# Kernel optimization log

Hardware: AMD Instinct MI355X
Metric: run time of the kernel (lower is better)

Reference implementation:

```python
import jax, jax.numpy as jnp
import numpy as np

BITS = 4
N_PACK = 8  # 32-bit container / 4-bit values
GROUPSIZE = 128
MASK = (1 << BITS) - 1


def _unpack(packed, n_valid):
    # packed: [R, ceil(n_valid/N_PACK)] int32 -> [R, n_valid] int32 nibbles
    shifts = (jnp.arange(N_PACK, dtype=jnp.int32) * BITS)
    vals = (packed[:, :, None] >> shifts) & MASK  # [R, C, N_PACK]
    return vals.reshape(packed.shape[0], -1)[:, :n_valid]


def setup_inputs() -> dict:
    key = jax.random.key(0)
    k0, k1, k2, k3, k4 = jax.random.split(key, 5)
    O, I = 4096, 4096
    ng = I // GROUPSIZE  # 32
    x = jax.random.normal(k0, (2, 2048, I), dtype=jnp.float32)
    packed_weight = jax.random.randint(k1, (O, I // N_PACK), 0, 2147483647, dtype=jnp.int32)
    scale = jax.random.uniform(k2, (O, ng), dtype=jnp.float32)
    packed_zp = jax.random.randint(k3, (O, (ng + N_PACK - 1) // N_PACK), 0, 2147483647, dtype=jnp.int32)
    bias = jax.random.normal(k4, (O,), dtype=jnp.float32)
    return {"x": x, "packed_weight": packed_weight, "scale": scale,
            "packed_zp": packed_zp, "bias": bias}


def reference(x, packed_weight, scale, packed_zp, bias):
    O, ng = scale.shape
    I = packed_weight.shape[1] * N_PACK
    # unpack uint4 weights and zero-points (matches torch recover(): shift+mask)
    w_int = _unpack(packed_weight, I)          # [O, I] values in [0, 15]
    zp_int = _unpack(packed_zp, ng)            # [O, ng]
    # per-group dequant: (w - zp) * scale
    w = w_int.reshape(O, ng, GROUPSIZE).astype(scale.dtype)
    fp_weight = ((w - zp_int[:, :, None].astype(scale.dtype)) * scale[:, :, None]).reshape(O, I)
    # F.linear: x @ W^T + b
    return jnp.einsum('bsi,oi->bso', x, fp_weight) + bias
```

## Files before the change

### kernel.cpp

```cpp
#include <hip/hip_runtime.h>
#include <stdint.h>

typedef __attribute__((ext_vector_type(4))) float  floatx4;
typedef __attribute__((ext_vector_type(8))) short  shortx8;
typedef __attribute__((ext_vector_type(4))) unsigned short ushortx4;

typedef unsigned int   u32;
typedef unsigned short u16;

#define TILE    128
#define BK      64
#define THREADS 256
#define CHUNK   (TILE * BK)

__device__ __forceinline__ u32 pack2bf(float f0, float f1) {
    u32 u0 = __builtin_bit_cast(u32, f0) + 0x8000u;
    u32 u1 = __builtin_bit_cast(u32, f1) + 0x8000u;
    return __builtin_amdgcn_perm(u1, u0, 0x07060302u);
}

__device__ __forceinline__ unsigned short f2bf(float f) {
    u32 u = __builtin_bit_cast(u32, f);
    u += 0x7FFFu + ((u >> 16) & 1u);
    return (unsigned short)(u >> 16);
}

__global__ __launch_bounds__(THREADS)
void prep_kernel(const float* __restrict__ x, const int* __restrict__ pw,
                 const float* __restrict__ scale, const int* __restrict__ pzp,
                 u16* __restrict__ At, u16* __restrict__ Bt,
                 int M, int O, int I, int ng, int KT) {
    const int bid = blockIdx.x;
    const int t   = threadIdx.x;
    if (bid < M * 2) {
        const int row  = bid >> 1;
        const int cseg = (bid & 1) * THREADS + t;
        const int kt = cseg >> 3, cp = cseg & 7;
        const int r = row & (TILE - 1), mt = row >> 7;
        const int c = cp ^ (r & 7);
        const float4 v0 = *(const float4*)(x + (size_t)row * I + kt * BK + c * 8);
        const float4 v1 = *(const float4*)(x + (size_t)row * I + kt * BK + c * 8 + 4);
        u32 p[4];
        p[0] = pack2bf(v0.x, v0.y);
        p[1] = pack2bf(v0.z, v0.w);
        p[2] = pack2bf(v1.x, v1.y);
        p[3] = pack2bf(v1.z, v1.w);
        *(uint4*)(At + (size_t)(mt * KT + kt) * CHUNK + r * BK + cp * 8) = *(uint4*)p;
    } else {
        const int bid2 = bid - M * 2;
        const int o    = bid2 >> 1;
        const int wpos = (bid2 & 1) * THREADS + t;
        const int kt = wpos >> 3, cp = wpos & 7;
        const int r = o & (TILE - 1), nt = o >> 7;
        const int c = cp ^ (r & 7);
        const u32 wq = (u32)pw[(size_t)o * (I >> 3) + kt * 8 + c];
        const int g  = (kt * BK) / (I / ng);
        const float s = scale[o * ng + g];
        const int zpw = pzp[o * ((ng + 7) >> 3) + (g >> 3)];
        const int zp  = (zpw >> ((g & 7) * 4)) & 15;
        const float nzc = -s * (float)(zp + 128);
        float v[8];
        #pragma unroll
        for (int j = 0; j < 8; j++) {
            u32 tt;
            if (j < 4)       tt = (wq << (16 - 4 * j)) & 0x000F0000u;
            else if (j == 4) tt = wq & 0x000F0000u;
            else             tt = (wq >> (4 * j - 16)) & 0x000F0000u;
            float f = __builtin_bit_cast(float, tt | 0x43000000u);
            v[j] = __builtin_fmaf(f, s, nzc);
        }
        u32 p[4];
        p[0] = pack2bf(v[0], v[1]);
        p[1] = pack2bf(v[2], v[3]);
        p[2] = pack2bf(v[4], v[5]);
        p[3] = pack2bf(v[6], v[7]);
        *(uint4*)(Bt + (size_t)(nt * KT + kt) * CHUNK + r * BK + cp * 8) = *(uint4*)p;
    }
}

__global__ __launch_bounds__(THREADS, 2)
void gemm_bf16(const u16* __restrict__ At, const u16* __restrict__ Bt,
               const float* __restrict__ bias, float* __restrict__ out,
               int O, int KT) {
    __shared__ u16 As[CHUNK];
    __shared__ u16 Bs[CHUNK];

    const int tid = threadIdx.x;
    const int nblk_n = O / TILE;
    const int mt = blockIdx.x / nblk_n;
    const int nt = blockIdx.x % nblk_n;
    const int w = tid >> 6, lane = tid & 63;
    const int wm = w >> 1, wn = w & 1;
    const int l15 = lane & 15, l4 = lane >> 4;
    const int sw  = l15 & 7;

    floatx4 acc[4][4];
    #pragma unroll
    for (int i = 0; i < 4; i++)
        #pragma unroll
        for (int j = 0; j < 4; j++)
            acc[i][j] = (floatx4){0.f, 0.f, 0.f, 0.f};

    for (int kt = 0; kt < KT; kt++) {
        const u16* ga = At + (size_t)(mt * KT + kt) * CHUNK;
        const u16* gb = Bt + (size_t)(nt * KT + kt) * CHUNK;
        __syncthreads();
        #pragma unroll
        for (int it = 0; it < 4; it++) {
            const int off = (it * THREADS + tid) * 8;
            __builtin_amdgcn_global_load_lds((const __attribute__((address_space(1))) u32*)(ga + off),
                                             (__attribute__((address_space(3))) u32*)(As + off),
                                             16, 0, 0);
            __builtin_amdgcn_global_load_lds((const __attribute__((address_space(1))) u32*)(gb + off),
                                             (__attribute__((address_space(3))) u32*)(Bs + off),
                                             16, 0, 0);
        }
        __syncthreads();

        #pragma unroll
        for (int ks = 0; ks < 2; ks++) {
            shortx8 af[4], bf[4];
            #pragma unroll
            for (int i = 0; i < 4; i++)
                af[i] = *(const shortx8*)(&As[(wm * 64 + i * 16 + l15) * BK + ((ks * 4 + l4) ^ sw) * 8]);
            #pragma unroll
            for (int j = 0; j < 4; j++)
                bf[j] = *(const shortx8*)(&Bs[(wn * 64 + j * 16 + l15) * BK + ((ks * 4 + l4) ^ sw) * 8]);
            #pragma unroll
            for (int i = 0; i < 4; i++)
                #pragma unroll
                for (int j = 0; j < 4; j++)
                    acc[i][j] = __builtin_amdgcn_mfma_f32_16x16x32_bf16(af[i], bf[j], acc[i][j], 0, 0, 0);
        }
    }

    #pragma unroll
    for (int j = 0; j < 4; j++) {
        int col  = nt * TILE + wn * 64 + j * 16 + l15;
        float bv = bias[col];
        #pragma unroll
        for (int i = 0; i < 4; i++) {
            int rowb = mt * TILE + wm * 64 + i * 16 + l4 * 4;
            #pragma unroll
            for (int r = 0; r < 4; r++)
                out[(size_t)(rowb + r) * O + col] = acc[i][j][r] + bv;
        }
    }
}

#define LDA 72
__global__ __launch_bounds__(THREADS, 2)
void wql_fused(const float* __restrict__ x, const int* __restrict__ pw,
               const float* __restrict__ scale, const int* __restrict__ pzp,
               const float* __restrict__ bias, float* __restrict__ out,
               int M, int O, int I, int ng)
{
    __shared__ unsigned short As[TILE * LDA];
    __shared__ unsigned short Bs[TILE * LDA];
    const int tid = threadIdx.x;
    const int nblk_n = O / TILE;
    const int mt = blockIdx.x / nblk_n, nt = blockIdx.x % nblk_n;
    const int w = tid >> 6, lane = tid & 63;
    const int wm = w >> 1, wn = w & 1;
    const int l15 = lane & 15, l4 = lane >> 4;
    const int pw_rowlen = I / 8, zp_rowlen = (ng + 7) / 8, GS = I / ng;

    floatx4 acc[4][4];
    #pragma unroll
    for (int i = 0; i < 4; i++)
        #pragma unroll
        for (int j = 0; j < 4; j++) acc[i][j] = (floatx4){0.f, 0.f, 0.f, 0.f};

    const int nk = I / BK;
    for (int kt = 0; kt < nk; kt++) {
        __syncthreads();
        #pragma unroll
        for (int it = 0; it < 8; it++) {
            int f = tid + it * THREADS;
            int row = f >> 4, seg = f & 15;
            const float4 v = *(const float4*)(x + (size_t)(mt * TILE + row) * I + kt * BK + seg * 4);
            ushortx4 b;
            b.x = f2bf(v.x); b.y = f2bf(v.y); b.z = f2bf(v.z); b.w = f2bf(v.w);
            *(ushortx4*)(&As[row * LDA + seg * 4]) = b;
        }
        const int g = (kt * BK) / GS;
        #pragma unroll
        for (int it = 0; it < 4; it++) {
            int e = tid + it * THREADS;
            int row = e >> 3, c = e & 7;
            int o = nt * TILE + row;
            int wq = pw[(size_t)o * pw_rowlen + kt * (BK / 8) + c];
            float s = scale[o * ng + g];
            int zpw = pzp[o * zp_rowlen + (g >> 3)];
            int zp = (zpw >> ((g & 7) * 4)) & 15;
            shortx8 b;
            #pragma unroll
            for (int j = 0; j < 8; j++) {
                int nib = (wq >> (4 * j)) & 15;
                b[j] = (short)f2bf((float)(nib - zp) * s);
            }
            *(shortx8*)(&Bs[row * LDA + c * 8]) = b;
        }
        __syncthreads();
        #pragma unroll
        for (int ks = 0; ks < 2; ks++) {
            shortx8 af[4], bf[4];
            #pragma unroll
            for (int i = 0; i < 4; i++)
                af[i] = *(const shortx8*)(&As[(wm * 64 + i * 16 + l15) * LDA + ks * 32 + l4 * 8]);
            #pragma unroll
            for (int j = 0; j < 4; j++)
                bf[j] = *(const shortx8*)(&Bs[(wn * 64 + j * 16 + l15) * LDA + ks * 32 + l4 * 8]);
            #pragma unroll
            for (int i = 0; i < 4; i++)
                #pragma unroll
                for (int j = 0; j < 4; j++)
                    acc[i][j] = __builtin_amdgcn_mfma_f32_16x16x32_bf16(af[i], bf[j], acc[i][j], 0, 0, 0);
        }
    }
    #pragma unroll
    for (int j = 0; j < 4; j++) {
        int col = nt * TILE + wn * 64 + j * 16 + l15;
        float bv = bias[col];
        #pragma unroll
        for (int i = 0; i < 4; i++) {
            int rowb = mt * TILE + wm * 64 + i * 16 + l4 * 4;
            #pragma unroll
            for (int r = 0; r < 4; r++)
                out[(size_t)(rowb + r) * O + col] = acc[i][j][r] + bv;
        }
    }
}

extern "C" void kernel_launch(void* const* d_in, const int* in_sizes, int n_in,
                              void* d_out, int out_size, void* d_ws, size_t ws_size,
                              hipStream_t stream) {
    const float* x     = (const float*)d_in[0];
    const int*   pw    = (const int*)d_in[1];
    const float* scale = (const float*)d_in[2];
    const int*   pzp   = (const int*)d_in[3];
    const float* bias  = (const float*)d_in[4];
    float*       out   = (float*)d_out;

    const int O  = in_sizes[4];
    const int ng = in_sizes[2] / O;
    const int I  = (in_sizes[1] / O) * 8;
    const int M  = in_sizes[0] / I;
    const int KT = I / BK;

    const size_t need = ((size_t)M * I + (size_t)O * I) * sizeof(u16);
    if (ws_size >= need) {
        u16* At = (u16*)d_ws;
        u16* Bt = At + (size_t)M * I;
        prep_kernel<<<dim3(M * 2 + O * 2), THREADS, 0, stream>>>(x, pw, scale, pzp, At, Bt, M, O, I, ng, KT);
        gemm_bf16<<<dim3((M / TILE) * (O / TILE)), THREADS, 0, stream>>>(At, Bt, bias, out, O, KT);
    } else {
        wql_fused<<<dim3((M / TILE) * (O / TILE)), THREADS, 0, stream>>>(x, pw, scale, pzp, bias, out, M, O, I, ng);
    }
}
```

Measured before the change: 257.6 us.

## Double-buffer GEMM LDS loads and use grid-stride prep kernel

Result: slower. 270.3 us (+4.9%).

```diff
diff --git a/kernel.cpp b/kernel.cpp
--- a/kernel.cpp
+++ b/kernel.cpp
@@ -29,36 +29,40 @@
 void prep_kernel(const float* __restrict__ x, const int* __restrict__ pw,
                  const float* __restrict__ scale, const int* __restrict__ pzp,
                  u16* __restrict__ At, u16* __restrict__ Bt,
-                 int M, int O, int I, int ng, int KT) {
-    const int bid = blockIdx.x;
-    const int t   = threadIdx.x;
-    if (bid < M * 2) {
-        const int row  = bid >> 1;
-        const int cseg = (bid & 1) * THREADS + t;
+                 int M, int O, int I, int ng, int KT, int lsSeg) {
+    const int NT = gridDim.x * THREADS;
+    const int t0 = blockIdx.x * THREADS + threadIdx.x;
+    const int segsPerRow = I >> 3;
+
+    const int Sx = M * segsPerRow;
+    for (int s = t0; s < Sx; s += NT) {
+        const int row = s >> lsSeg;
+        const int cseg = s & (segsPerRow - 1);
         const int kt = cseg >> 3, cp = cseg & 7;
         const int r = row & (TILE - 1), mt = row >> 7;
         const int c = cp ^ (r & 7);
         const float4 v0 = *(const float4*)(x + (size_t)row * I + kt * BK + c * 8);
         const float4 v1 = *(const float4*)(x + (size_t)row * I + kt * BK + c * 8 + 4);
         u32 p[4];
-        p[0] = pack2bf(v0.x, v0.y);
-        p[1] = pack2bf(v0.z, v0.w);
-        p[2] = pack2bf(v1.x, v1.y);
-        p[3] = pack2bf(v1.z, v1.w);
+        p[0] = pack2bf(v0.x, v0.y); p[1] = pack2bf(v0.z, v0.w);
+        p[2] = pack2bf(v1.x, v1.y); p[3] = pack2bf(v1.z, v1.w);
         *(uint4*)(At + (size_t)(mt * KT + kt) * CHUNK + r * BK + cp * 8) = *(uint4*)p;
-    } else {
-        const int bid2 = bid - M * 2;
-        const int o    = bid2 >> 1;
-        const int wpos = (bid2 & 1) * THREADS + t;
+    }
+
+    const int GS = I / ng;
+    const int Sw = O * segsPerRow;
+    for (int s = t0; s < Sw; s += NT) {
+        const int o = s >> lsSeg;
+        const int wpos = s & (segsPerRow - 1);
         const int kt = wpos >> 3, cp = wpos & 7;
         const int r = o & (TILE - 1), nt = o >> 7;
         const int c = cp ^ (r & 7);
-        const u32 wq = (u32)pw[(size_t)o * (I >> 3) + kt * 8 + c];
-        const int g  = (kt * BK) / (I / ng);
-        const float s = scale[o * ng + g];
+        const u32 wq = (u32)pw[(size_t)o * segsPerRow + kt * 8 + c];
+        const int g = (kt * BK) / GS;
+        const float sc = scale[o * ng + g];
         const int zpw = pzp[o * ((ng + 7) >> 3) + (g >> 3)];
-        const int zp  = (zpw >> ((g & 7) * 4)) & 15;
-        const float nzc = -s * (float)(zp + 128);
+        const int zp = (zpw >> ((g & 7) * 4)) & 15;
+        const float nzc = -sc * (float)(zp + 128);
         float v[8];
         #pragma unroll
         for (int j = 0; j < 8; j++) {
@@ -66,14 +70,11 @@
             if (j < 4)       tt = (wq << (16 - 4 * j)) & 0x000F0000u;
             else if (j == 4) tt = wq & 0x000F0000u;
             else             tt = (wq >> (4 * j - 16)) & 0x000F0000u;
-            float f = __builtin_bit_cast(float, tt | 0x43000000u);
-            v[j] = __builtin_fmaf(f, s, nzc);
+            v[j] = __builtin_fmaf(__builtin_bit_cast(float, tt | 0x43000000u), sc, nzc);
         }
         u32 p[4];
-        p[0] = pack2bf(v[0], v[1]);
-        p[1] = pack2bf(v[2], v[3]);
-        p[2] = pack2bf(v[4], v[5]);
-        p[3] = pack2bf(v[6], v[7]);
+        p[0] = pack2bf(v[0], v[1]); p[1] = pack2bf(v[2], v[3]);
+        p[2] = pack2bf(v[4], v[5]); p[3] = pack2bf(v[6], v[7]);
         *(uint4*)(Bt + (size_t)(nt * KT + kt) * CHUNK + r * BK + cp * 8) = *(uint4*)p;
     }
 }
@@ -82,8 +83,10 @@
 void gemm_bf16(const u16* __restrict__ At, const u16* __restrict__ Bt,
                const float* __restrict__ bias, float* __restrict__ out,
                int O, int KT) {
-    __shared__ u16 As[CHUNK];
-    __shared__ u16 Bs[CHUNK];
+    __shared__ u16 As0[CHUNK];
+    __shared__ u16 Bs0[CHUNK];
+    __shared__ u16 As1[CHUNK];
+    __shared__ u16 Bs1[CHUNK];
 
     const int tid = threadIdx.x;
     const int nblk_n = O / TILE;
@@ -101,38 +104,60 @@
         for (int j = 0; j < 4; j++)
             acc[i][j] = (floatx4){0.f, 0.f, 0.f, 0.f};
 
-    for (int kt = 0; kt < KT; kt++) {
-        const u16* ga = At + (size_t)(mt * KT + kt) * CHUNK;
-        const u16* gb = Bt + (size_t)(nt * KT + kt) * CHUNK;
-        __syncthreads();
-        #pragma unroll
-        for (int it = 0; it < 4; it++) {
-            const int off = (it * THREADS + tid) * 8;
-            __builtin_amdgcn_global_load_lds((const __attribute__((address_space(1))) u32*)(ga + off),
-                                             (__attribute__((address_space(3))) u32*)(As + off),
-                                             16, 0, 0);
-            __builtin_amdgcn_global_load_lds((const __attribute__((address_space(1))) u32*)(gb + off),
-                                             (__attribute__((address_space(3))) u32*)(Bs + off),
-                                             16, 0, 0);
-        }
-        __syncthreads();
-
-        #pragma unroll
-        for (int ks = 0; ks < 2; ks++) {
-            shortx8 af[4], bf[4];
-            #pragma unroll
-            for (int i = 0; i < 4; i++)
-                af[i] = *(const shortx8*)(&As[(wm * 64 + i * 16 + l15) * BK + ((ks * 4 + l4) ^ sw) * 8]);
-            #pragma unroll
-            for (int j = 0; j < 4; j++)
-                bf[j] = *(const shortx8*)(&Bs[(wn * 64 + j * 16 + l15) * BK + ((ks * 4 + l4) ^ sw) * 8]);
-            #pragma unroll
-            for (int i = 0; i < 4; i++)
-                #pragma unroll
-                for (int j = 0; j < 4; j++)
-                    acc[i][j] = __builtin_amdgcn_mfma_f32_16x16x32_bf16(af[i], bf[j], acc[i][j], 0, 0, 0);
-        }
-    }
+#define ISSUE(KTI, AS_, BS_) do {                                                              \
+    const u16* ga_ = At + (size_t)(mt * KT + (KTI)) * CHUNK;                                   \
+    const u16* gb_ = Bt + (size_t)(nt * KT + (KTI)) * CHUNK;                                   \
+    _Pragma("unroll")                                                                          \
+    for (int it_ = 0; it_ < 4; it_++) {                                                        \
+        const int off_ = (it_ * THREADS + tid) * 8;                                            \
+        __builtin_amdgcn_global_load_lds((const __attribute__((address_space(1))) u32*)(ga_ + off_), \
+                                         (__attribute__((address_space(3))) u32*)(AS_ + off_), 16, 0, 0); \
+        __builtin_amdgcn_global_load_lds((const __attribute__((address_space(1))) u32*)(gb_ + off_), \
+                                         (__attribute__((address_space(3))) u32*)(BS_ + off_), 16, 0, 0); \
+    }                                                                                          \
+} while (0)
+
+#define COMPUTE(AS_, BS_) do {                                                                 \
+    _Pragma("unroll")                                                                          \
+    for (int ks_ = 0; ks_ < 2; ks_++) {                                                        \
+        shortx8 af_[4], bf_[4];                                                                \
+        _Pragma("unroll")                                                                      \
+        for (int i_ = 0; i_ < 4; i_++)                                                         \
+            af_[i_] = *(const shortx8*)(&AS_[(wm * 64 + i_ * 16 + l15) * BK + ((ks_ * 4 + l4) ^ sw) * 8]); \
+        _Pragma("unroll")                                                                      \
+        for (int j_ = 0; j_ < 4; j_++)                                                         \
+            bf_[j_] = *(const shortx8*)(&BS_[(wn * 64 + j_ * 16 + l15) * BK + ((ks_ * 4 + l4) ^ sw) * 8]); \
+        _Pragma("unroll")                                                                      \
+        for (int i_ = 0; i_ < 4; i_++)                                                         \
+            _Pragma("unroll")                                                                  \
+            for (int j_ = 0; j_ < 4; j_++)                                                     \
+                acc[i_][j_] = __builtin_amdgcn_mfma_f32_16x16x32_bf16(af_[i_], bf_[j_], acc[i_][j_], 0, 0, 0); \
+    }                                                                                          \
+} while (0)
+
+#define WAITBAR8() __asm__ volatile("s_waitcnt vmcnt(8)\n\ts_barrier" ::: "memory")
+#define WAITBAR0() __asm__ volatile("s_waitcnt vmcnt(0)\n\ts_barrier" ::: "memory")
+#define ENDBAR()   __asm__ volatile("s_waitcnt lgkmcnt(0)\n\ts_barrier" ::: "memory")
+
+    ISSUE(0, As0, Bs0);
+    for (int kt = 0; kt < KT; kt += 2) {
+        if (kt + 1 < KT) { ISSUE(kt + 1, As1, Bs1); WAITBAR8(); }
+        else             { WAITBAR0(); }
+        COMPUTE(As0, Bs0);
+        ENDBAR();
+        if (kt + 1 < KT) {
+            if (kt + 2 < KT) { ISSUE(kt + 2, As0, Bs0); WAITBAR8(); }
+            else             { WAITBAR0(); }
+            COMPUTE(As1, Bs1);
+            ENDBAR();
+        }
+    }
+
+#undef ISSUE
+#undef COMPUTE
+#undef WAITBAR8
+#undef WAITBAR0
+#undef ENDBAR
 
     #pragma unroll
     for (int j = 0; j < 4; j++) {
@@ -247,12 +272,13 @@
     const int I  = (in_sizes[1] / O) * 8;
     const int M  = in_sizes[0] / I;
     const int KT = I / BK;
+    int lsSeg = 0; { int v = I >> 3; while ((1 << lsSeg) < v) lsSeg++; }
 
     const size_t need = ((size_t)M * I + (size_t)O * I) * sizeof(u16);
     if (ws_size >= need) {
         u16* At = (u16*)d_ws;
         u16* Bt = At + (size_t)M * I;
-        prep_kernel<<<dim3(M * 2 + O * 2), THREADS, 0, stream>>>(x, pw, scale, pzp, At, Bt, M, O, I, ng, KT);
+        prep_kernel<<<dim3(2048), THREADS, 0, stream>>>(x, pw, scale, pzp, At, Bt, M, O, I, ng, KT, lsSeg);
         gemm_bf16<<<dim3((M / TILE) * (O / TILE)), THREADS, 0, stream>>>(At, Bt, bias, out, O, KT);
     } else {
         wql_fused<<<dim3((M / TILE) * (O / TILE)), THREADS, 0, stream>>>(x, pw, scale, pzp, bias, out, M, O, I, ng);
```

## Store prepped operands row-major and apply swizzle during GEMM tile loads

Applied to the files above, without the earlier changes.

Result: no change. 257.2 us (-0.1%).

```diff
diff --git a/kernel.cpp b/kernel.cpp
--- a/kernel.cpp
+++ b/kernel.cpp
@@ -29,36 +29,31 @@
 void prep_kernel(const float* __restrict__ x, const int* __restrict__ pw,
                  const float* __restrict__ scale, const int* __restrict__ pzp,
                  u16* __restrict__ At, u16* __restrict__ Bt,
-                 int M, int O, int I, int ng, int KT) {
-    const int bid = blockIdx.x;
-    const int t   = threadIdx.x;
-    if (bid < M * 2) {
-        const int row  = bid >> 1;
-        const int cseg = (bid & 1) * THREADS + t;
-        const int kt = cseg >> 3, cp = cseg & 7;
-        const int r = row & (TILE - 1), mt = row >> 7;
-        const int c = cp ^ (r & 7);
-        const float4 v0 = *(const float4*)(x + (size_t)row * I + kt * BK + c * 8);
-        const float4 v1 = *(const float4*)(x + (size_t)row * I + kt * BK + c * 8 + 4);
+                 int M, int O, int I, int ng, int lsSeg, int lsG) {
+    const int NT = gridDim.x * THREADS;
+    const int t0 = blockIdx.x * THREADS + threadIdx.x;
+    const int segsPerRow = I >> 3;
+
+    const int Sx = (M * I) >> 3;
+    for (int s = t0; s < Sx; s += NT) {
+        const float4 v0 = ((const float4*)x)[(size_t)s * 2];
+        const float4 v1 = ((const float4*)x)[(size_t)s * 2 + 1];
         u32 p[4];
-        p[0] = pack2bf(v0.x, v0.y);
-        p[1] = pack2bf(v0.z, v0.w);
-        p[2] = pack2bf(v1.x, v1.y);
-        p[3] = pack2bf(v1.z, v1.w);
-        *(uint4*)(At + (size_t)(mt * KT + kt) * CHUNK + r * BK + cp * 8) = *(uint4*)p;
-    } else {
-        const int bid2 = bid - M * 2;
-        const int o    = bid2 >> 1;
-        const int wpos = (bid2 & 1) * THREADS + t;
-        const int kt = wpos >> 3, cp = wpos & 7;
-        const int r = o & (TILE - 1), nt = o >> 7;
-        const int c = cp ^ (r & 7);
-        const u32 wq = (u32)pw[(size_t)o * (I >> 3) + kt * 8 + c];
-        const int g  = (kt * BK) / (I / ng);
-        const float s = scale[o * ng + g];
-        const int zpw = pzp[o * ((ng + 7) >> 3) + (g >> 3)];
-        const int zp  = (zpw >> ((g & 7) * 4)) & 15;
-        const float nzc = -s * (float)(zp + 128);
+        p[0] = pack2bf(v0.x, v0.y); p[1] = pack2bf(v0.z, v0.w);
+        p[2] = pack2bf(v1.x, v1.y); p[3] = pack2bf(v1.z, v1.w);
+        ((uint4*)At)[s] = *(uint4*)p;
+    }
+
+    const int Sw = (O * I) >> 3;
+    for (int s = t0; s < Sw; s += NT) {
+        const u32 wq = (u32)pw[s];
+        const int o    = s >> lsSeg;
+        const int wcol = s & (segsPerRow - 1);
+        const int g    = wcol >> lsG;
+        const float sc = scale[o * ng + g];
+        const int zpw  = pzp[o * ((ng + 7) >> 3) + (g >> 3)];
+        const int zp   = (zpw >> ((g & 7) * 4)) & 15;
+        const float nzc = -sc * (float)(zp + 128);
         float v[8];
         #pragma unroll
         for (int j = 0; j < 8; j++) {
@@ -66,22 +61,19 @@
             if (j < 4)       tt = (wq << (16 - 4 * j)) & 0x000F0000u;
             else if (j == 4) tt = wq & 0x000F0000u;
             else             tt = (wq >> (4 * j - 16)) & 0x000F0000u;
-            float f = __builtin_bit_cast(float, tt | 0x43000000u);
-            v[j] = __builtin_fmaf(f, s, nzc);
+            v[j] = __builtin_fmaf(__builtin_bit_cast(float, tt | 0x43000000u), sc, nzc);
         }
         u32 p[4];
-        p[0] = pack2bf(v[0], v[1]);
-        p[1] = pack2bf(v[2], v[3]);
-        p[2] = pack2bf(v[4], v[5]);
-        p[3] = pack2bf(v[6], v[7]);
-        *(uint4*)(Bt + (size_t)(nt * KT + kt) * CHUNK + r * BK + cp * 8) = *(uint4*)p;
+        p[0] = pack2bf(v[0], v[1]); p[1] = pack2bf(v[2], v[3]);
+        p[2] = pack2bf(v[4], v[5]); p[3] = pack2bf(v[6], v[7]);
+        ((uint4*)Bt)[s] = *(uint4*)p;
     }
 }
 
 __global__ __launch_bounds__(THREADS, 2)
 void gemm_bf16(const u16* __restrict__ At, const u16* __restrict__ Bt,
                const float* __restrict__ bias, float* __restrict__ out,
-               int O, int KT) {
+               int O, int I, int KT) {
     __shared__ u16 As[CHUNK];
     __shared__ u16 Bs[CHUNK];
 
@@ -94,6 +86,9 @@
     const int l15 = lane & 15, l4 = lane >> 4;
     const int sw  = l15 & 7;
 
+    const int sr = tid >> 3;
+    const int sc = (tid & 7) ^ (sr & 7);
+
     floatx4 acc[4][4];
     #pragma unroll
     for (int i = 0; i < 4; i++)
@@ -101,18 +96,22 @@
         for (int j = 0; j < 4; j++)
             acc[i][j] = (floatx4){0.f, 0.f, 0.f, 0.f};
 
+    const u16* gaBase = At + ((size_t)(mt * TILE) + sr) * I + sc * 8;
+    const u16* gbBase = Bt + ((size_t)(nt * TILE) + sr) * I + sc * 8;
+
     for (int kt = 0; kt < KT; kt++) {
-        const u16* ga = At + (size_t)(mt * KT + kt) * CHUNK;
-        const u16* gb = Bt + (size_t)(nt * KT + kt) * CHUNK;
+        const u16* ga = gaBase + kt * BK;
+        const u16* gb = gbBase + kt * BK;
         __syncthreads();
         #pragma unroll
         for (int it = 0; it < 4; it++) {
-            const int off = (it * THREADS + tid) * 8;
-            __builtin_amdgcn_global_load_lds((const __attribute__((address_space(1))) u32*)(ga + off),
-                                             (__attribute__((address_space(3))) u32*)(As + off),
+            const int ldsOff = it * 2048 + tid * 8;
+            const size_t gOff = (size_t)(it * 32) * I;
+            __builtin_amdgcn_global_load_lds((const __attribute__((address_space(1))) u32*)(ga + gOff),
+                                             (__attribute__((address_space(3))) u32*)(As + ldsOff),
                                              16, 0, 0);
-            __builtin_amdgcn_global_load_lds((const __attribute__((address_space(1))) u32*)(gb + off),
-                                             (__attribute__((address_space(3))) u32*)(Bs + off),
+            __builtin_amdgcn_global_load_lds((const __attribute__((address_space(1))) u32*)(gb + gOff),
+                                             (__attribute__((address_space(3))) u32*)(Bs + ldsOff),
                                              16, 0, 0);
         }
         __syncthreads();
@@ -247,13 +246,15 @@
     const int I  = (in_sizes[1] / O) * 8;
     const int M  = in_sizes[0] / I;
     const int KT = I / BK;
+    int lsSeg = 0; { int v = I >> 3; while ((1 << lsSeg) < v) lsSeg++; }
+    int lsG = 0;   { int v = (I / ng) >> 3; while ((1 << lsG) < v) lsG++; }
 
     const size_t need = ((size_t)M * I + (size_t)O * I) * sizeof(u16);
     if (ws_size >= need) {
         u16* At = (u16*)d_ws;
         u16* Bt = At + (size_t)M * I;
-        prep_kernel<<<dim3(M * 2 + O * 2), THREADS, 0, stream>>>(x, pw, scale, pzp, At, Bt, M, O, I, ng, KT);
-        gemm_bf16<<<dim3((M / TILE) * (O / TILE)), THREADS, 0, stream>>>(At, Bt, bias, out, O, KT);
+        prep_kernel<<<dim3(2048), THREADS, 0, stream>>>(x, pw, scale, pzp, At, Bt, M, O, I, ng, lsSeg, lsG);
+        gemm_bf16<<<dim3((M / TILE) * (O / TILE)), THREADS, 0, stream>>>(At, Bt, bias, out, O, I, KT);
     } else {
         wql_fused<<<dim3((M / TILE) * (O / TILE)), THREADS, 0, stream>>>(x, pw, scale, pzp, bias, out, M, O, I, ng);
     }
```
